# Performance work log

Measured on AMD Instinct MI355X. Metric: run time of the kernel, lower is better.

The kernel has to match this reference:

```python
import jax, jax.numpy as jnp
import numpy as np

N = 8192
IN_C = 256
OUT_C = 64
ALPHA = 0.2  # LeakyReLU negative slope
NEG_INF = -9e15


def setup_inputs() -> dict:
    key = jax.random.key(0)
    k1, k2, k3, k4 = jax.random.split(key, 4)
    x = jax.random.normal(k1, (N, IN_C), dtype=jnp.float32)
    adjacent = jax.random.randint(k2, (N, N), 0, 2, dtype=jnp.int32)
    # xavier_uniform with gain=1.2: limit = gain * sqrt(6/(fan_in+fan_out))
    lim_w = 1.2 * np.sqrt(6.0 / (IN_C + OUT_C))
    w = jax.random.uniform(k3, (IN_C, OUT_C), dtype=jnp.float32, minval=-lim_w, maxval=lim_w)
    lim_a = 1.2 * np.sqrt(6.0 / (2 * OUT_C + 1))
    a = jax.random.uniform(k4, (2 * OUT_C, 1), dtype=jnp.float32, minval=-lim_a, maxval=lim_a)
    return {"x": x, "adjacent": adjacent, "w": w, "a": a}


def reference(x, adjacent, w, a):
    # h: [N, out]
    h = x @ w
    # e_ij = LeakyReLU(a^T [h_i || h_j]) computed without materializing [N,N,2*out]:
    # split a into source/target halves -> rank-1 broadcast sum.
    a_src = a[:OUT_C, 0]   # [out]
    a_dst = a[OUT_C:, 0]   # [out]
    f_src = h @ a_src      # [N]
    f_dst = h @ a_dst      # [N]
    e = f_src[:, None] + f_dst[None, :]            # [N, N]
    e = jnp.where(e > 0, e, ALPHA * e)             # LeakyReLU
    # mask by adjacency, softmax over neighbors (rows)
    e = jnp.where(adjacent > 0, e, NEG_INF)
    attention = jax.nn.softmax(e, axis=-1)         # [N, N]
    h_prime = attention @ h                        # [N, out]
    # concat=True -> ELU activation
    return jax.nn.elu(h_prime)
```

## Files before the change

kernel.cpp:

```cpp
#include <hip/hip_runtime.h>
#include <hip/hip_bf16.h>

#define N 8192
#define IN_C 256
#define OUT_C 64
#define ALPHA 0.2f

typedef short bf16x8 __attribute__((ext_vector_type(8)));
typedef float f32x4 __attribute__((ext_vector_type(4)));

#define OFF_H      0u
#define OFF_HT     2097152u
#define OFF_FS     3145728u
#define OFF_FD     3178496u
#define OFF_FDMAX  3211264u
#define OFF_NUM    3211520u
#define OFF_DEN    11600128u

__global__ __launch_bounds__(256) void k_linear(const float* __restrict__ x,
                                                const float* __restrict__ w,
                                                float* __restrict__ h) {
    __shared__ float wl[IN_C * OUT_C];
    int t = threadIdx.x;
    for (int idx = t; idx < IN_C * OUT_C; idx += 256) wl[idx] = w[idx];
    __syncthreads();
    int i = blockIdx.x * 4 + (t >> 6);
    int c = t & 63;
    const float* xr = x + (size_t)i * IN_C;
    float acc = 0.f;
#pragma unroll 8
    for (int k = 0; k < IN_C; ++k) acc = fmaf(xr[k], wl[k * 64 + c], acc);
    h[(size_t)i * 64 + c] = acc;
}

__global__ __launch_bounds__(256) void k_tr(const float* __restrict__ h,
                                            __hip_bfloat16* __restrict__ ht) {
    __shared__ __hip_bfloat16 lds[64 * 65];
    int t = threadIdx.x;
    int i0 = blockIdx.x * 64;
#pragma unroll
    for (int k = 0; k < 16; ++k) {
        int idx = k * 256 + t;
        int il = idx >> 6, c = idx & 63;
        lds[c * 65 + il] = __float2bfloat16(h[(size_t)(i0 + il) * 64 + c]);
    }
    __syncthreads();
#pragma unroll
    for (int k = 0; k < 16; ++k) {
        int idx = k * 256 + t;
        int c = idx >> 6, il = idx & 63;
        ht[(size_t)c * N + i0 + il] = lds[c * 65 + il];
    }
}

__global__ __launch_bounds__(256) void k_f(const float* __restrict__ h,
                                           const float* __restrict__ a,
                                           float* __restrict__ fs,
                                           float* __restrict__ fd) {
    int t = threadIdx.x;
    int lane = t & 63;
    int i = blockIdx.x * 4 + (t >> 6);
    float v = h[(size_t)i * 64 + lane];
    float s = v * a[lane];
    float d = v * a[64 + lane];
#pragma unroll
    for (int off = 32; off > 0; off >>= 1) {
        s += __shfl_xor(s, off, 64);
        d += __shfl_xor(d, off, 64);
    }
    if (lane == 0) { fs[i] = s; fd[i] = d; }
}

__global__ __launch_bounds__(256) void k_fdmax(const float* __restrict__ fd,
                                               float* __restrict__ out) {
    __shared__ float red[256];
    int t = threadIdx.x;
    float m = -3.4e38f;
    for (int j = t; j < N; j += 256) m = fmaxf(m, fd[j]);
    red[t] = m;
    __syncthreads();
    for (int s = 128; s > 0; s >>= 1) {
        if (t < s) red[t] = fmaxf(red[t], red[t + s]);
        __syncthreads();
    }
    if (t == 0) out[0] = red[0];
}

__global__ __launch_bounds__(256, 2) void k_main(
    const int* __restrict__ adj,
    const float* __restrict__ fsrc,
    const float* __restrict__ fdst,
    const float* __restrict__ fdmax_p,
    const unsigned short* __restrict__ ht,
    float* __restrict__ nump,
    float* __restrict__ denp_out) {
    int bid = blockIdx.x;
    int rb = bid >> 2;
    int kq = bid & 3;
    int t = threadIdx.x;
    int wave = t >> 6;
    int lane = t & 63;
    int r  = lane & 15;
    int kg = lane >> 4;
    int i  = rb * 64 + wave * 16 + r;
    int j0 = kq * 2048;

    float fs  = fsrc[i];
    float fdm = *fdmax_p;
    float e0  = fs + fdm;
    float m   = fmaxf(e0, ALPHA * e0);

    const int* arow = adj + (size_t)i * N;
    f32x4 acc0 = {0.f, 0.f, 0.f, 0.f};
    f32x4 acc1 = {0.f, 0.f, 0.f, 0.f};
    f32x4 acc2 = {0.f, 0.f, 0.f, 0.f};
    f32x4 acc3 = {0.f, 0.f, 0.f, 0.f};
    float dacc = 0.f;

#pragma unroll 2
    for (int ks = 0; ks < 64; ++ks) {
        int jb = j0 + ks * 32 + kg * 8;
        int4   ad0 = *(const int4*)(arow + jb);
        int4   ad1 = *(const int4*)(arow + jb + 4);
        float4 fd0 = *(const float4*)(fdst + jb);
        float4 fd1 = *(const float4*)(fdst + jb + 4);
        bf16x8 b0 = *(const bf16x8*)(ht + (size_t)(0 * 16 + r) * N + jb);
        bf16x8 b1 = *(const bf16x8*)(ht + (size_t)(1 * 16 + r) * N + jb);
        bf16x8 b2 = *(const bf16x8*)(ht + (size_t)(2 * 16 + r) * N + jb);
        bf16x8 b3 = *(const bf16x8*)(ht + (size_t)(3 * 16 + r) * N + jb);

        int   ad[8]  = {ad0.x, ad0.y, ad0.z, ad0.w, ad1.x, ad1.y, ad1.z, ad1.w};
        float fdv[8] = {fd0.x, fd0.y, fd0.z, fd0.w, fd1.x, fd1.y, fd1.z, fd1.w};
        bf16x8 af;
#pragma unroll
        for (int e = 0; e < 8; ++e) {
            float ee = fs + fdv[e];
            float l  = fmaxf(ee, ALPHA * ee);
            float wt = (ad[e] > 0) ? __expf(l - m) : 0.f;
            dacc += wt;
            union { float f; unsigned u; } cv; cv.f = wt;
            unsigned ru = cv.u + 0x7FFF + ((cv.u >> 16) & 1);
            af[e] = (short)(ru >> 16);
        }
        acc0 = __builtin_amdgcn_mfma_f32_16x16x32_bf16(af, b0, acc0, 0, 0, 0);
        acc1 = __builtin_amdgcn_mfma_f32_16x16x32_bf16(af, b1, acc1, 0, 0, 0);
        acc2 = __builtin_amdgcn_mfma_f32_16x16x32_bf16(af, b2, acc2, 0, 0, 0);
        acc3 = __builtin_amdgcn_mfma_f32_16x16x32_bf16(af, b3, acc3, 0, 0, 0);
    }

    dacc += __shfl_xor(dacc, 16, 64);
    dacc += __shfl_xor(dacc, 32, 64);
    if (kg == 0) denp_out[kq * N + i] = dacc;

    int orow = rb * 64 + wave * 16 + kg * 4;
    float* np = nump + (size_t)kq * N * 64;
#pragma unroll
    for (int rr = 0; rr < 4; ++rr) {
        np[(size_t)(orow + rr) * 64 + 0 * 16 + r] = acc0[rr];
        np[(size_t)(orow + rr) * 64 + 1 * 16 + r] = acc1[rr];
        np[(size_t)(orow + rr) * 64 + 2 * 16 + r] = acc2[rr];
        np[(size_t)(orow + rr) * 64 + 3 * 16 + r] = acc3[rr];
    }
}

__global__ __launch_bounds__(256) void k_final(const float* __restrict__ nump,
                                               const float* __restrict__ denp,
                                               float* __restrict__ out) {
    int gid = blockIdx.x * 256 + threadIdx.x;
    int i = gid >> 6;
    float num = nump[gid] + nump[524288 + gid] + nump[2 * 524288 + gid] + nump[3 * 524288 + gid];
    float den = denp[i] + denp[N + i] + denp[2 * N + i] + denp[3 * N + i];
    float v = num / den;
    out[gid] = v > 0.f ? v : __expf(v) - 1.f;
}

extern "C" void kernel_launch(void* const* d_in, const int* in_sizes, int n_in,
                              void* d_out, int out_size, void* d_ws, size_t ws_size,
                              hipStream_t stream) {
    const float* x   = (const float*)d_in[0];
    const int*   adj = (const int*)d_in[1];
    const float* w   = (const float*)d_in[2];
    const float* a   = (const float*)d_in[3];
    float* out = (float*)d_out;
    char*  ws  = (char*)d_ws;

    float*          h    = (float*)(ws + OFF_H);
    __hip_bfloat16* ht   = (__hip_bfloat16*)(ws + OFF_HT);
    float*          fs   = (float*)(ws + OFF_FS);
    float*          fd   = (float*)(ws + OFF_FD);
    float*          fdm  = (float*)(ws + OFF_FDMAX);
    float*          nump = (float*)(ws + OFF_NUM);
    float*          denp = (float*)(ws + OFF_DEN);

    k_linear<<<2048, 256, 0, stream>>>(x, w, h);
    k_tr<<<128, 256, 0, stream>>>(h, ht);
    k_f<<<2048, 256, 0, stream>>>(h, a, fs, fd);
    k_fdmax<<<1, 256, 0, stream>>>(fd, fdm);
    k_main<<<512, 256, 0, stream>>>(adj, fs, fd, fdm, (const unsigned short*)ht, nump, denp);
    k_final<<<2048, 256, 0, stream>>>(nump, denp, out);
}
```

Before: 560.5 us.

## Double-buffer main loop loads, split K into more chunks, fuse score projection

The main attention kernel now uses explicit two-stage register double buffering, so the loads for the next 32-column step are issued before the current step's compute. This hides global memory latency on the adjacency and transposed-feature streams. The column range is split into 8 chunks instead of 4 when workspace allows, doubling the block count for better occupancy, and block indexing puts the row-block in the low bits. The source/destination score projection is fused into the linear kernel, removing one launch. The cost is higher register pressure, since the launch-bounds occupancy hint is dropped, plus more partial sums for the final reduction to read.

```diff
diff --git a/kernel.cpp b/kernel.cpp
--- a/kernel.cpp
+++ b/kernel.cpp
@@ -15,11 +15,13 @@
 #define OFF_FD     3178496u
 #define OFF_FDMAX  3211264u
 #define OFF_NUM    3211520u
-#define OFF_DEN    11600128u
 
 __global__ __launch_bounds__(256) void k_linear(const float* __restrict__ x,
                                                 const float* __restrict__ w,
-                                                float* __restrict__ h) {
+                                                const float* __restrict__ a,
+                                                float* __restrict__ h,
+                                                float* __restrict__ fs,
+                                                float* __restrict__ fd) {
     __shared__ float wl[IN_C * OUT_C];
     int t = threadIdx.x;
     for (int idx = t; idx < IN_C * OUT_C; idx += 256) wl[idx] = w[idx];
@@ -31,6 +33,14 @@
 #pragma unroll 8
     for (int k = 0; k < IN_C; ++k) acc = fmaf(xr[k], wl[k * 64 + c], acc);
     h[(size_t)i * 64 + c] = acc;
+    float s = acc * a[c];
+    float d = acc * a[64 + c];
+#pragma unroll
+    for (int off = 32; off > 0; off >>= 1) {
+        s += __shfl_xor(s, off, 64);
+        d += __shfl_xor(d, off, 64);
+    }
+    if (c == 0) { fs[i] = s; fd[i] = d; }
 }
 
 __global__ __launch_bounds__(256) void k_tr(const float* __restrict__ h,
@@ -51,24 +61,6 @@
         int c = idx >> 6, il = idx & 63;
         ht[(size_t)c * N + i0 + il] = lds[c * 65 + il];
     }
-}
-
-__global__ __launch_bounds__(256) void k_f(const float* __restrict__ h,
-                                           const float* __restrict__ a,
-                                           float* __restrict__ fs,
-                                           float* __restrict__ fd) {
-    int t = threadIdx.x;
-    int lane = t & 63;
-    int i = blockIdx.x * 4 + (t >> 6);
-    float v = h[(size_t)i * 64 + lane];
-    float s = v * a[lane];
-    float d = v * a[64 + lane];
-#pragma unroll
-    for (int off = 32; off > 0; off >>= 1) {
-        s += __shfl_xor(s, off, 64);
-        d += __shfl_xor(d, off, 64);
-    }
-    if (lane == 0) { fs[i] = s; fd[i] = d; }
 }
 
 __global__ __launch_bounds__(256) void k_fdmax(const float* __restrict__ fd,
@@ -86,24 +78,67 @@
     if (t == 0) out[0] = red[0];
 }
 
-__global__ __launch_bounds__(256, 2) void k_main(
+struct Stage {
+    int4   ad0, ad1;
+    float4 fd0, fd1;
+    bf16x8 b0, b1, b2, b3;
+};
+
+__device__ __forceinline__ void load_stage(Stage& s,
+        const int* __restrict__ arow, const float* __restrict__ fdst,
+        const unsigned short* __restrict__ pb0, const unsigned short* __restrict__ pb1,
+        const unsigned short* __restrict__ pb2, const unsigned short* __restrict__ pb3,
+        int jb) {
+    s.ad0 = *(const int4*)(arow + jb);
+    s.ad1 = *(const int4*)(arow + jb + 4);
+    s.fd0 = *(const float4*)(fdst + jb);
+    s.fd1 = *(const float4*)(fdst + jb + 4);
+    s.b0  = *(const bf16x8*)(pb0 + jb);
+    s.b1  = *(const bf16x8*)(pb1 + jb);
+    s.b2  = *(const bf16x8*)(pb2 + jb);
+    s.b3  = *(const bf16x8*)(pb3 + jb);
+}
+
+__device__ __forceinline__ void compute_stage(const Stage& s, float fs, float m,
+        float& dacc, f32x4& acc0, f32x4& acc1, f32x4& acc2, f32x4& acc3) {
+    int   ad[8]  = {s.ad0.x, s.ad0.y, s.ad0.z, s.ad0.w, s.ad1.x, s.ad1.y, s.ad1.z, s.ad1.w};
+    float fdv[8] = {s.fd0.x, s.fd0.y, s.fd0.z, s.fd0.w, s.fd1.x, s.fd1.y, s.fd1.z, s.fd1.w};
+    bf16x8 af;
+#pragma unroll
+    for (int e = 0; e < 8; ++e) {
+        float ee = fs + fdv[e];
+        float l  = fmaxf(ee, ALPHA * ee);
+        float wt = (ad[e] > 0) ? __expf(l - m) : 0.f;
+        dacc += wt;
+        union { float f; unsigned u; } cv; cv.f = wt;
+        unsigned ru = cv.u + 0x7FFF + ((cv.u >> 16) & 1);
+        af[e] = (short)(ru >> 16);
+    }
+    acc0 = __builtin_amdgcn_mfma_f32_16x16x32_bf16(af, s.b0, acc0, 0, 0, 0);
+    acc1 = __builtin_amdgcn_mfma_f32_16x16x32_bf16(af, s.b1, acc1, 0, 0, 0);
+    acc2 = __builtin_amdgcn_mfma_f32_16x16x32_bf16(af, s.b2, acc2, 0, 0, 0);
+    acc3 = __builtin_amdgcn_mfma_f32_16x16x32_bf16(af, s.b3, acc3, 0, 0, 0);
+}
+
+__global__ __launch_bounds__(256) void k_main(
     const int* __restrict__ adj,
     const float* __restrict__ fsrc,
     const float* __restrict__ fdst,
     const float* __restrict__ fdmax_p,
     const unsigned short* __restrict__ ht,
     float* __restrict__ nump,
-    float* __restrict__ denp_out) {
+    float* __restrict__ denp_out,
+    int jch, int ns) {
     int bid = blockIdx.x;
-    int rb = bid >> 2;
-    int kq = bid & 3;
+    int rb = bid & 127;
+    int kq = bid >> 7;
     int t = threadIdx.x;
     int wave = t >> 6;
     int lane = t & 63;
     int r  = lane & 15;
     int kg = lane >> 4;
     int i  = rb * 64 + wave * 16 + r;
-    int j0 = kq * 2048;
+    int j0 = kq * jch;
 
     float fs  = fsrc[i];
     float fdm = *fdmax_p;
@@ -111,42 +146,29 @@
     float m   = fmaxf(e0, ALPHA * e0);
 
     const int* arow = adj + (size_t)i * N;
-    f32x4 acc0 = {0.f, 0.f, 0.f, 0.f};
-    f32x4 acc1 = {0.f, 0.f, 0.f, 0.f};
-    f32x4 acc2 = {0.f, 0.f, 0.f, 0.f};
-    f32x4 acc3 = {0.f, 0.f, 0.f, 0.f};
+    const unsigned short* pb0 = ht + (size_t)(r)      * N;
+    const unsigned short* pb1 = ht + (size_t)(16 + r) * N;
+    const unsigned short* pb2 = ht + (size_t)(32 + r) * N;
+    const unsigned short* pb3 = ht + (size_t)(48 + r) * N;
+
+    f32x4 acc0 = {0.f,0.f,0.f,0.f}, acc1 = {0.f,0.f,0.f,0.f};
+    f32x4 acc2 = {0.f,0.f,0.f,0.f}, acc3 = {0.f,0.f,0.f,0.f};
     float dacc = 0.f;
 
-#pragma unroll 2
-    for (int ks = 0; ks < 64; ++ks) {
-        int jb = j0 + ks * 32 + kg * 8;
-        int4   ad0 = *(const int4*)(arow + jb);
-        int4   ad1 = *(const int4*)(arow + jb + 4);
-        float4 fd0 = *(const float4*)(fdst + jb);
-        float4 fd1 = *(const float4*)(fdst + jb + 4);
-        bf16x8 b0 = *(const bf16x8*)(ht + (size_t)(0 * 16 + r) * N + jb);
-        bf16x8 b1 = *(const bf16x8*)(ht + (size_t)(1 * 16 + r) * N + jb);
-        bf16x8 b2 = *(const bf16x8*)(ht + (size_t)(2 * 16 + r) * N + jb);
-        bf16x8 b3 = *(const bf16x8*)(ht + (size_t)(3 * 16 + r) * N + jb);
-
-        int   ad[8]  = {ad0.x, ad0.y, ad0.z, ad0.w, ad1.x, ad1.y, ad1.z, ad1.w};
-        float fdv[8] = {fd0.x, fd0.y, fd0.z, fd0.w, fd1.x, fd1.y, fd1.z, fd1.w};
-        bf16x8 af;
-#pragma unroll
-        for (int e = 0; e < 8; ++e) {
-            float ee = fs + fdv[e];
-            float l  = fmaxf(ee, ALPHA * ee);
-            float wt = (ad[e] > 0) ? __expf(l - m) : 0.f;
-            dacc += wt;
-            union { float f; unsigned u; } cv; cv.f = wt;
-            unsigned ru = cv.u + 0x7FFF + ((cv.u >> 16) & 1);
-            af[e] = (short)(ru >> 16);
-        }
-        acc0 = __builtin_amdgcn_mfma_f32_16x16x32_bf16(af, b0, acc0, 0, 0, 0);
-        acc1 = __builtin_amdgcn_mfma_f32_16x16x32_bf16(af, b1, acc1, 0, 0, 0);
-        acc2 = __builtin_amdgcn_mfma_f32_16x16x32_bf16(af, b2, acc2, 0, 0, 0);
-        acc3 = __builtin_amdgcn_mfma_f32_16x16x32_bf16(af, b3, acc3, 0, 0, 0);
-    }
+    int base = j0 + kg * 8;
+    Stage A, B;
+    load_stage(A, arow, fdst, pb0, pb1, pb2, pb3, base);
+    load_stage(B, arow, fdst, pb0, pb1, pb2, pb3, base + 32);
+
+#pragma unroll 1
+    for (int ks = 0; ks < ns - 2; ks += 2) {
+        compute_stage(A, fs, m, dacc, acc0, acc1, acc2, acc3);
+        load_stage(A, arow, fdst, pb0, pb1, pb2, pb3, base + (ks + 2) * 32);
+        compute_stage(B, fs, m, dacc, acc0, acc1, acc2, acc3);
+        load_stage(B, arow, fdst, pb0, pb1, pb2, pb3, base + (ks + 3) * 32);
+    }
+    compute_stage(A, fs, m, dacc, acc0, acc1, acc2, acc3);
+    compute_stage(B, fs, m, dacc, acc0, acc1, acc2, acc3);
 
     dacc += __shfl_xor(dacc, 16, 64);
     dacc += __shfl_xor(dacc, 32, 64);
@@ -165,11 +187,15 @@
 
 __global__ __launch_bounds__(256) void k_final(const float* __restrict__ nump,
                                                const float* __restrict__ denp,
-                                               float* __restrict__ out) {
+                                               float* __restrict__ out,
+                                               int kqn) {
     int gid = blockIdx.x * 256 + threadIdx.x;
     int i = gid >> 6;
-    float num = nump[gid] + nump[524288 + gid] + nump[2 * 524288 + gid] + nump[3 * 524288 + gid];
-    float den = denp[i] + denp[N + i] + denp[2 * N + i] + denp[3 * N + i];
+    float num = 0.f, den = 0.f;
+    for (int q = 0; q < kqn; ++q) {
+        num += nump[(size_t)q * (N * 64) + gid];
+        den += denp[q * N + i];
+    }
     float v = num / den;
     out[gid] = v > 0.f ? v : __expf(v) - 1.f;
 }
@@ -190,12 +216,17 @@
     float*          fd   = (float*)(ws + OFF_FD);
     float*          fdm  = (float*)(ws + OFF_FDMAX);
     float*          nump = (float*)(ws + OFF_NUM);
-    float*          denp = (float*)(ws + OFF_DEN);
-
-    k_linear<<<2048, 256, 0, stream>>>(x, w, h);
+
+    size_t need8 = (size_t)OFF_NUM + 8ull * N * 64 * 4 + 8ull * N * 4;
+    int KQ = (ws_size >= need8) ? 8 : 4;
+    float* denp = nump + (size_t)KQ * N * 64;
+    int jch = N / KQ;
+    int ns  = jch / 32;
+
+    k_linear<<<2048, 256, 0, stream>>>(x, w, a, h, fs, fd);
     k_tr<<<128, 256, 0, stream>>>(h, ht);
-    k_f<<<2048, 256, 0, stream>>>(h, a, fs, fd);
     k_fdmax<<<1, 256, 0, stream>>>(fd, fdm);
-    k_main<<<512, 256, 0, stream>>>(adj, fs, fd, fdm, (const unsigned short*)ht, nump, denp);
-    k_final<<<2048, 256, 0, stream>>>(nump, denp, out);
-}
+    k_main<<<KQ * 128, 256, 0, stream>>>(adj, fs, fd, fdm,
+                                         (const unsigned short*)ht, nump, denp, jch, ns);
+    k_final<<<2048, 256, 0, stream>>>(nump, denp, out, KQ);
+}
```

After: 469.9 us. -16.2%, faster.
